# Kernel tuning notes

Measured on AMD Instinct MI355X. Metric: run time of the kernel, lower is better.

The kernel has to match this reference:

```python
import jax, jax.numpy as jnp
import numpy as np
from jax import lax

V, E, H, S = 50000, 512, 512, 16384


def setup_inputs() -> dict:
    key = jax.random.key(0)
    ks = jax.random.split(key, 10)
    sc_e = 1.0 / np.sqrt(E)
    sc_h = 1.0 / np.sqrt(H)
    return {
        "x": jax.random.randint(ks[0], (S,), 0, V, dtype=jnp.int64)
        if jax.config.jax_enable_x64
        else jax.random.randint(ks[0], (S,), 0, V, dtype=jnp.int32),
        "emb_table": jax.random.normal(ks[1], (V, E), dtype=jnp.float32),
        "W_ih": jax.random.uniform(ks[2], (4 * H, E), jnp.float32, -sc_h, sc_h),
        "W_hh": jax.random.uniform(ks[3], (4 * H, H), jnp.float32, -sc_h, sc_h),
        "b_ih": jax.random.uniform(ks[4], (4 * H,), jnp.float32, -sc_h, sc_h),
        "b_hh": jax.random.uniform(ks[5], (4 * H,), jnp.float32, -sc_h, sc_h),
        "W1": jax.random.uniform(ks[6], (128, H), jnp.float32, -sc_h, sc_h),
        "b1": jax.random.uniform(ks[7], (128,), jnp.float32, -sc_h, sc_h),
        "W2": jax.random.uniform(ks[8], (9, 128), jnp.float32, -1 / np.sqrt(128), 1 / np.sqrt(128)),
        "b2": jax.random.uniform(ks[9], (9,), jnp.float32, -1 / np.sqrt(128), 1 / np.sqrt(128)),
    }


def reference(x, emb_table, W_ih, W_hh, b_ih, b_hh, W1, b1, W2, b2):
    # Embedding lookup: [S, E]  (batch=1 via view(1,-1,E) in the original)
    w2v = emb_table[x]
    # Precompute input contributions to the 4 gates for all timesteps: [S, 4H]
    gx = w2v @ W_ih.T + (b_ih + b_hh)

    def step(carry, gxt):
        h, c = carry
        g = gxt + h @ W_hh.T  # [4H]; torch gate order: i, f, g, o
        i = jax.nn.sigmoid(g[:H])
        f = jax.nn.sigmoid(g[H : 2 * H])
        gg = jnp.tanh(g[2 * H : 3 * H])
        o = jax.nn.sigmoid(g[3 * H :])
        c = f * c + i * gg
        h = o * jnp.tanh(c)
        return (h, c), None

    h0 = jnp.zeros((H,), dtype=w2v.dtype)
    c0 = jnp.zeros((H,), dtype=w2v.dtype)
    (h_last, _), _ = lax.scan(step, (h0, c0), gx)

    out = jax.nn.sigmoid(h_last @ W1.T + b1)
    out = jax.nn.sigmoid(out @ W2.T + b2)
    return out[None, :]  # [1, 9], matching out[:, -1, :] batch dim
```

## Files before the change

kernel.cpp:

```cpp
#include <hip/hip_runtime.h>
#include <hip/hip_bf16.h>


#define S_LEN 16384
#define NWG   16
#define NLAUNCH 256
#define NTHR  512

typedef unsigned long long u64;
typedef float float4v __attribute__((ext_vector_type(4)));

static __device__ __forceinline__ float bf2f(unsigned int u16) {
  union { unsigned int i; float f; } v; v.i = u16 << 16; return v.f;
}
static __device__ __forceinline__ unsigned short f2bf(float f) {
  union { float f; unsigned int i; } v; v.f = f;
  unsigned int r = v.i + 0x7fffu + ((v.i >> 16) & 1u);
  return (unsigned short)(r >> 16);
}
static __device__ __forceinline__ float fsig(float x) { return 1.f / (1.f + __expf(-x)); }
static __device__ __forceinline__ float ftanh(float x) { return 2.f / (1.f + __expf(-2.f * x)) - 1.f; }

static __device__ __forceinline__ int haddr(int k) { return k + (k >> 4); }

__global__ __launch_bounds__(256, 2) void gx_gemm(
    const int* __restrict__ x, const float* __restrict__ emb,
    const float* __restrict__ W_ih, const float* __restrict__ b_ih,
    const float* __restrict__ b_hh, unsigned short* __restrict__ gx)
{
  __shared__ float As[64][40];
  __shared__ float Bs[64][40];
  __shared__ int   xs[64];

  const int tid = threadIdx.x;
  const int bm = blockIdx.x;
  const int bn = blockIdx.y;

  if (tid < 64) xs[tid] = x[bm * 64 + tid];
  __syncthreads();

  float acc[4][4] = {};
  const int r0 = (tid >> 4) * 4;
  const int c0 = tid & 15;

  for (int kc = 0; kc < 512; kc += 32) {
#pragma unroll
    for (int h = 0; h < 2; ++h) {
      const int v = tid + h * 256;
      const int row = v >> 3, k4 = v & 7;
      const float4 av = *(const float4*)(emb + (size_t)xs[row] * 512 + kc + k4 * 4);
      As[row][k4 * 4 + 0] = av.x; As[row][k4 * 4 + 1] = av.y;
      As[row][k4 * 4 + 2] = av.z; As[row][k4 * 4 + 3] = av.w;
      const float4 bv = *(const float4*)(W_ih + (size_t)(bn * 64 + row) * 512 + kc + k4 * 4);
      Bs[row][k4 * 4 + 0] = bv.x; Bs[row][k4 * 4 + 1] = bv.y;
      Bs[row][k4 * 4 + 2] = bv.z; Bs[row][k4 * 4 + 3] = bv.w;
    }
    __syncthreads();
#pragma unroll
    for (int k4 = 0; k4 < 8; ++k4) {
      float4 a[4], b[4];
#pragma unroll
      for (int i = 0; i < 4; ++i) a[i] = *(const float4*)&As[r0 + i][k4 * 4];
#pragma unroll
      for (int j = 0; j < 4; ++j) b[j] = *(const float4*)&Bs[c0 + j * 16][k4 * 4];
#pragma unroll
      for (int i = 0; i < 4; ++i)
#pragma unroll
        for (int j = 0; j < 4; ++j) {
          acc[i][j] = __builtin_fmaf(a[i].x, b[j].x, acc[i][j]);
          acc[i][j] = __builtin_fmaf(a[i].y, b[j].y, acc[i][j]);
          acc[i][j] = __builtin_fmaf(a[i].z, b[j].z, acc[i][j]);
          acc[i][j] = __builtin_fmaf(a[i].w, b[j].w, acc[i][j]);
        }
    }
    __syncthreads();
  }

#pragma unroll
  for (int j = 0; j < 4; ++j) {
    const int c = bn * 64 + c0 + j * 16;
    const float bias = b_ih[c] + b_hh[c];
    const size_t dstc = (size_t)(c & 511) * 4 + (size_t)(c >> 9);
#pragma unroll
    for (int i = 0; i < 4; ++i) {
      const size_t t = (size_t)bm * 64 + r0 + i;
      gx[t * 2048 + dstc] = f2bf(acc[i][j] + bias);
    }
  }
}

__global__ __launch_bounds__(NTHR, 1) void lstm_rec(
    const float* __restrict__ W_hh, const unsigned short* __restrict__ gx,
    const float* __restrict__ W1, const float* __restrict__ b1,
    const float* __restrict__ W2, const float* __restrict__ b2,
    float* __restrict__ out,
    u64* __restrict__ h_glob,
    unsigned int* __restrict__ done)
{
  const int tid = threadIdx.x;
  const int w   = blockIdx.x;

  if (w >= NWG) {
    float a0 = (float)tid, a1 = a0 + 1.f, a2 = a0 + 2.f, a3 = a0 + 3.f;
    for (;;) {
      if (__hip_atomic_load(done, __ATOMIC_RELAXED, __HIP_MEMORY_SCOPE_AGENT))
        break;
#pragma unroll 32
      for (int i = 0; i < 512; ++i) {
        a0 = __builtin_fmaf(a0, 1.0000001f, 1e-9f);
        a1 = __builtin_fmaf(a1, 0.9999999f, 1e-9f);
        a2 = __builtin_fmaf(a2, 1.0000002f, 1e-9f);
        a3 = __builtin_fmaf(a3, 0.9999998f, 1e-9f);
      }
    }
    asm volatile("" :: "v"(a0), "v"(a1), "v"(a2), "v"(a3));
    return;
  }

  const int s    = tid & 31;
  const int half = (tid >> 5) & 1;
  const int wvi  = tid >> 6;
  const int ubase  = w * 32 + wvi * 4 + half * 2;
  const int ulocal = wvi * 4 + half * 2;

  float4v wvv[32];
#pragma unroll
  for (int q = 0; q < 8; ++q) {
    const int row = (q & 3) * 512 + ubase + (q >> 2);
    const float* src = W_hh + (size_t)row * 512 + s * 16;
#pragma unroll
    for (int i4 = 0; i4 < 4; ++i4) {
      asm volatile("global_load_dwordx4 %0, %1, off\n\ts_waitcnt vmcnt(0)"
                   : "=v"(wvv[q * 4 + i4]) : "v"((u64)(src + i4 * 4)) : "memory");
    }
  }

  __shared__ float hbuf[2][544];
  __shared__ u64   stage[32];

  float c0 = 0.f, c1 = 0.f;
  float h_reg[16];
#pragma unroll
  for (int i = 0; i < 16; ++i) h_reg[i] = 0.f;

  uint4 g_cur = {0,0,0,0}, g_nxt = {0,0,0,0};
  if (s == 0) {
    g_cur = *(const uint4*)(gx + (size_t)0 * 2048 + ubase * 4);
    g_nxt = *(const uint4*)(gx + (size_t)1 * 2048 + ubase * 4);
  }

  for (int t = 0; t < S_LEN; ++t) {
    uint4 g_new = {0,0,0,0};
    if (s == 0 && t + 2 < S_LEN)
      g_new = *(const uint4*)(gx + (size_t)(t + 2) * 2048 + ubase * 4);

    float acc[8];
#pragma unroll
    for (int q = 0; q < 8; ++q) {
      float a = 0.f;
#pragma unroll
      for (int i4 = 0; i4 < 4; ++i4) {
        const float4v vv = wvv[q * 4 + i4];
        a = __builtin_fmaf(vv.x, h_reg[i4 * 4 + 0], a);
        a = __builtin_fmaf(vv.y, h_reg[i4 * 4 + 1], a);
        a = __builtin_fmaf(vv.z, h_reg[i4 * 4 + 2], a);
        a = __builtin_fmaf(vv.w, h_reg[i4 * 4 + 3], a);
      }
      acc[q] = a;
    }
#pragma unroll
    for (int q = 0; q < 8; ++q) {
      float a = acc[q];
      a += __shfl_xor(a, 1);
      a += __shfl_xor(a, 2);
      a += __shfl_xor(a, 4);
      a += __shfl_xor(a, 8);
      a += __shfl_xor(a, 16);
      acc[q] = a;
    }

    const int buf = (t + 1) & 1;
    if (s == 0) {
      const float pi0 = acc[0] + bf2f(g_cur.x & 0xffffu);
      const float pf0 = acc[1] + bf2f(g_cur.x >> 16);
      const float pg0 = acc[2] + bf2f(g_cur.y & 0xffffu);
      const float po0 = acc[3] + bf2f(g_cur.y >> 16);
      const float pi1 = acc[4] + bf2f(g_cur.z & 0xffffu);
      const float pf1 = acc[5] + bf2f(g_cur.z >> 16);
      const float pg1 = acc[6] + bf2f(g_cur.w & 0xffffu);
      const float po1 = acc[7] + bf2f(g_cur.w >> 16);
      c0 = fsig(pf0) * c0 + fsig(pi0) * ftanh(pg0);
      c1 = fsig(pf1) * c1 + fsig(pi1) * ftanh(pg1);
      const float h0 = fsig(po0) * ftanh(c0);
      const float h1 = fsig(po1) * ftanh(c1);
      union { float f; unsigned int u; } a0, a1; a0.f = h0; a1.f = h1;
      const u64 tg = (u64)(unsigned)(t + 1) << 32;
      ulonglong2 pk;
      pk.x = tg | (u64)a0.u;
      pk.y = tg | (u64)a1.u;
      *(ulonglong2*)&stage[ulocal] = pk;
    }
    __syncthreads();

    if (tid < 64) {
      if (tid < 16) {
        __hip_atomic_store(&h_glob[buf * 512 + w * 32 + tid], stage[tid],
                           __ATOMIC_RELAXED, __HIP_MEMORY_SCOPE_AGENT);
        __hip_atomic_store(&h_glob[buf * 512 + w * 32 + 16 + tid], stage[tid + 16],
                           __ATOMIC_RELAXED, __HIP_MEMORY_SCOPE_AGENT);
      }
      if (t + 1 < S_LEN) {
        const u64* hb = h_glob + buf * 512;
        const unsigned want = (unsigned)(t + 1);
        u64 v[8];
        for (;;) {
#pragma unroll
          for (int i = 0; i < 8; ++i)
            v[i] = __hip_atomic_load(&hb[i * 64 + tid],
                                     __ATOMIC_RELAXED, __HIP_MEMORY_SCOPE_AGENT);
          bool ok = true;
#pragma unroll
          for (int i = 0; i < 8; ++i) ok &= ((unsigned)(v[i] >> 32) >= want);
          if (__all(ok)) break;
        }
#pragma unroll
        for (int i = 0; i < 8; ++i) {
          union { unsigned int u; float f; } hu; hu.u = (unsigned)v[i];
          hbuf[buf][haddr(i * 64 + tid)] = hu.f;
        }
      }
    }
    __syncthreads();

    if (t + 1 < S_LEN) {
      const int base = s * 17;
#pragma unroll
      for (int i = 0; i < 16; ++i)
        h_reg[i] = hbuf[buf][base + i];
    }

    g_cur = g_nxt; g_nxt = g_new;
  }

  if (w == 0 && tid == 0)
    __hip_atomic_store(done, 1u, __ATOMIC_RELAXED, __HIP_MEMORY_SCOPE_AGENT);

  if (w == 0) {
    __shared__ float hl[512];
    __shared__ float zl[128];
    {
      u64 v;
      do {
        v = __hip_atomic_load(&h_glob[tid], __ATOMIC_RELAXED, __HIP_MEMORY_SCOPE_AGENT);
      } while ((unsigned)(v >> 32) < (unsigned)S_LEN);
      union { unsigned int u; float f; } hu; hu.u = (unsigned)v;
      hl[tid] = hu.f;
    }
    __syncthreads();
    const int j = tid >> 2, q = tid & 3;
    float sum = 0.f;
    const float4* w1v = (const float4*)(W1 + (size_t)j * 512 + q * 128);
#pragma unroll 8
    for (int k4 = 0; k4 < 32; ++k4) {
      const float4 v = w1v[k4];
      const int kb = q * 128 + k4 * 4;
      sum = __builtin_fmaf(v.x, hl[kb + 0], sum);
      sum = __builtin_fmaf(v.y, hl[kb + 1], sum);
      sum = __builtin_fmaf(v.z, hl[kb + 2], sum);
      sum = __builtin_fmaf(v.w, hl[kb + 3], sum);
    }
    sum += __shfl_xor(sum, 1);
    sum += __shfl_xor(sum, 2);
    if (q == 0) zl[j] = fsig(sum + b1[j]);
    __syncthreads();
    if (tid < 9) {
      float o = b2[tid];
      const float* w2r = W2 + tid * 128;
#pragma unroll 16
      for (int k = 0; k < 128; ++k) o = __builtin_fmaf(w2r[k], zl[k], o);
      out[tid] = fsig(o);
    }
  }
}

extern "C" void kernel_launch(void* const* d_in, const int* in_sizes, int n_in,
                              void* d_out, int out_size, void* d_ws, size_t ws_size,
                              hipStream_t stream) {
  const int*   x     = (const int*)d_in[0];
  const float* emb   = (const float*)d_in[1];
  const float* W_ih  = (const float*)d_in[2];
  const float* W_hh  = (const float*)d_in[3];
  const float* b_ih  = (const float*)d_in[4];
  const float* b_hh  = (const float*)d_in[5];
  const float* W1    = (const float*)d_in[6];
  const float* b1    = (const float*)d_in[7];
  const float* W2    = (const float*)d_in[8];
  const float* b2    = (const float*)d_in[9];
  float* out = (float*)d_out;

  const size_t gx_bytes = (size_t)S_LEN * 2048 * sizeof(unsigned short);
  const size_t h_off    = gx_bytes;
  const size_t dn_off   = h_off + 8192;
  if (ws_size < h_off + 16384) return;

  unsigned short* gxp    = (unsigned short*)d_ws;
  u64*            h_glob = (u64*)((char*)d_ws + h_off);
  unsigned int*   done   = (unsigned int*)((char*)d_ws + dn_off);

  (void)hipMemsetAsync((char*)d_ws + h_off, 0, 16384, stream);

  dim3 g1(S_LEN / 64, 2048 / 64);
  gx_gemm<<<g1, 256, 0, stream>>>(x, emb, W_ih, b_ih, b_hh, gxp);
  lstm_rec<<<NLAUNCH, NTHR, 0, stream>>>(W_hh, gxp, W1, b1, W2, b2, out,
                                         h_glob, done);
}
```

Baseline: 44.51 ms.

## Pack bf16 hidden state with 16-bit step tags and drop staging barrier

Each hidden value is now stored as a 32-bit word holding a bf16 value and a 16-bit step tag. The writer lanes publish two units directly with one 64-bit atomic store, which removes the shared-memory staging buffer and one __syncthreads per timestep. The cross-workgroup exchange moves half the bytes, so each polling lane does 4 loads instead of 8. In exchange the recurrent hidden state is rounded to bf16 each step, which may add error over 16384 steps. The 16-bit tag wraps, and an equality check is used in place of >=.

```diff
diff --git a/kernel.cpp b/kernel.cpp
--- a/kernel.cpp
+++ b/kernel.cpp
@@ -94,7 +94,7 @@
     const float* __restrict__ W1, const float* __restrict__ b1,
     const float* __restrict__ W2, const float* __restrict__ b2,
     float* __restrict__ out,
-    u64* __restrict__ h_glob,
+    unsigned int* __restrict__ h32,
     unsigned int* __restrict__ done)
 {
   const int tid = threadIdx.x;
@@ -136,7 +136,6 @@
   }
 
   __shared__ float hbuf[2][544];
-  __shared__ u64   stage[32];
 
   float c0 = 0.f, c1 = 0.f;
   float h_reg[16];
@@ -193,41 +192,40 @@
       c1 = fsig(pf1) * c1 + fsig(pi1) * ftanh(pg1);
       const float h0 = fsig(po0) * ftanh(c0);
       const float h1 = fsig(po1) * ftanh(c1);
-      union { float f; unsigned int u; } a0, a1; a0.f = h0; a1.f = h1;
-      const u64 tg = (u64)(unsigned)(t + 1) << 32;
-      ulonglong2 pk;
-      pk.x = tg | (u64)a0.u;
-      pk.y = tg | (u64)a1.u;
-      *(ulonglong2*)&stage[ulocal] = pk;
-    }
-    __syncthreads();
-
-    if (tid < 64) {
-      if (tid < 16) {
-        __hip_atomic_store(&h_glob[buf * 512 + w * 32 + tid], stage[tid],
-                           __ATOMIC_RELAXED, __HIP_MEMORY_SCOPE_AGENT);
-        __hip_atomic_store(&h_glob[buf * 512 + w * 32 + 16 + tid], stage[tid + 16],
-                           __ATOMIC_RELAXED, __HIP_MEMORY_SCOPE_AGENT);
+      const unsigned tg16 = (unsigned)(t + 1) << 16;
+      const unsigned w0 = tg16 | (unsigned)f2bf(h0);
+      const unsigned w1 = tg16 | (unsigned)f2bf(h1);
+      const u64 pk = ((u64)w1 << 32) | (u64)w0;
+      __hip_atomic_store((u64*)&h32[buf * 512 + w * 32 + ulocal], pk,
+                         __ATOMIC_RELAXED, __HIP_MEMORY_SCOPE_AGENT);
+    }
+
+    if (tid < 64 && t + 1 < S_LEN) {
+      const u64* hb = (const u64*)(h32 + buf * 512);
+      const unsigned want = (unsigned)(t + 1) & 0xffffu;
+      u64 v[4];
+      for (;;) {
+#pragma unroll
+        for (int j = 0; j < 4; ++j)
+          v[j] = __hip_atomic_load(&hb[j * 64 + tid],
+                                   __ATOMIC_RELAXED, __HIP_MEMORY_SCOPE_AGENT);
+        bool ok = true;
+#pragma unroll
+        for (int j = 0; j < 4; ++j) {
+          ok &= (((unsigned)(v[j] >> 16) & 0xffffu) == want);
+          ok &= ((unsigned)(v[j] >> 48) == want);
+        }
+        if (__all(ok)) break;
       }
-      if (t + 1 < S_LEN) {
-        const u64* hb = h_glob + buf * 512;
-        const unsigned want = (unsigned)(t + 1);
-        u64 v[8];
-        for (;;) {
-#pragma unroll
-          for (int i = 0; i < 8; ++i)
-            v[i] = __hip_atomic_load(&hb[i * 64 + tid],
-                                     __ATOMIC_RELAXED, __HIP_MEMORY_SCOPE_AGENT);
-          bool ok = true;
-#pragma unroll
-          for (int i = 0; i < 8; ++i) ok &= ((unsigned)(v[i] >> 32) >= want);
-          if (__all(ok)) break;
-        }
-#pragma unroll
-        for (int i = 0; i < 8; ++i) {
-          union { unsigned int u; float f; } hu; hu.u = (unsigned)v[i];
-          hbuf[buf][haddr(i * 64 + tid)] = hu.f;
-        }
+#pragma unroll
+      for (int j = 0; j < 4; ++j) {
+        const int k = (j * 64 + tid) * 2;
+        const unsigned lo = (unsigned)v[j];
+        const unsigned hi = (unsigned)(v[j] >> 32);
+        union { unsigned u; float f; } f0, f1;
+        f0.u = lo << 16; f1.u = hi << 16;
+        hbuf[buf][haddr(k)]     = f0.f;
+        hbuf[buf][haddr(k + 1)] = f1.f;
       }
     }
     __syncthreads();
@@ -249,11 +247,11 @@
     __shared__ float hl[512];
     __shared__ float zl[128];
     {
-      u64 v;
+      unsigned v;
       do {
-        v = __hip_atomic_load(&h_glob[tid], __ATOMIC_RELAXED, __HIP_MEMORY_SCOPE_AGENT);
-      } while ((unsigned)(v >> 32) < (unsigned)S_LEN);
-      union { unsigned int u; float f; } hu; hu.u = (unsigned)v;
+        v = __hip_atomic_load(&h32[tid], __ATOMIC_RELAXED, __HIP_MEMORY_SCOPE_AGENT);
+      } while ((v >> 16) != (unsigned)S_LEN);
+      union { unsigned u; float f; } hu; hu.u = v << 16;
       hl[tid] = hu.f;
     }
     __syncthreads();
@@ -303,14 +301,14 @@
   const size_t dn_off   = h_off + 8192;
   if (ws_size < h_off + 16384) return;
 
-  unsigned short* gxp    = (unsigned short*)d_ws;
-  u64*            h_glob = (u64*)((char*)d_ws + h_off);
-  unsigned int*   done   = (unsigned int*)((char*)d_ws + dn_off);
+  unsigned short* gxp  = (unsigned short*)d_ws;
+  unsigned int*   h32  = (unsigned int*)((char*)d_ws + h_off);
+  unsigned int*   done = (unsigned int*)((char*)d_ws + dn_off);
 
   (void)hipMemsetAsync((char*)d_ws + h_off, 0, 16384, stream);
 
   dim3 g1(S_LEN / 64, 2048 / 64);
   gx_gemm<<<g1, 256, 0, stream>>>(x, emb, W_ih, b_ih, b_hh, gxp);
   lstm_rec<<<NLAUNCH, NTHR, 0, stream>>>(W_hh, gxp, W1, b1, W2, b2, out,
-                                         h_glob, done);
-}
+                                         h32, done);
+}
```

New measurement: 47.94 ms. 7.7% more time.
